# Performance work log

Measured on AMD Instinct MI355X. Metric: run time of the kernel, lower is better.

Reference implementation:

```python
import jax, jax.numpy as jnp
import numpy as np

B, CIN, COUT, H, W = 8, 128, 256, 256, 256


def setup_inputs() -> dict:
    key = jax.random.key(0)
    ks = jax.random.split(key, 6)
    x = jax.random.normal(ks[0], (B, CIN, H, W), dtype=jnp.float32)
    # conv weight [out, in, 3, 3]
    weight = jax.random.normal(ks[1], (COUT, CIN, 3, 3), dtype=jnp.float32) * 0.1
    move0_bias = jax.random.normal(ks[2], (1, CIN, 1, 1), dtype=jnp.float32) * 0.01
    pr_bias0 = jax.random.normal(ks[3], (1, COUT, 1, 1), dtype=jnp.float32) * 0.01
    prelu_alpha = jnp.full((COUT,), 0.25, dtype=jnp.float32)  # PyTorch PReLU default init
    pr_bias1 = jax.random.normal(ks[4], (1, COUT, 1, 1), dtype=jnp.float32) * 0.01
    return {"x": x, "weight": weight, "move0_bias": move0_bias,
            "pr_bias0": pr_bias0, "prelu_alpha": prelu_alpha, "pr_bias1": pr_bias1}


def _binary_activation(x):
    # STE: forward sign(x), backward grad of clip(x, -1, 1)
    clipped = jnp.clip(x, -1.0, 1.0)
    return jax.lax.stop_gradient(jnp.sign(x) - clipped) + clipped


def _binarize_weights(w):
    # per-output-filter scale: mean |w| over (in, kh, kw), detached
    scale = jax.lax.stop_gradient(jnp.mean(jnp.abs(w), axis=(1, 2, 3), keepdims=True))
    clipped = jnp.clip(w, -1.0, 1.0)
    return jax.lax.stop_gradient(scale * jnp.sign(w) - clipped) + clipped


def reference(x, weight, move0_bias, pr_bias0, prelu_alpha, pr_bias1):
    b, c, h, w = x.shape
    # AvgPool2d(kernel=2, stride=2)
    out = x.reshape(b, c, h // 2, 2, w // 2, 2).mean(axis=(3, 5))
    # LearnableBias
    out = out + move0_bias
    # BinaryActivation (sign with STE)
    out = _binary_activation(out)
    # HardBinaryConv 3x3, pad 1, stride 1, no bias
    bw = _binarize_weights(weight)
    y = jax.lax.conv_general_dilated(
        out, bw, window_strides=(1, 1), padding=((1, 1), (1, 1)),
        dimension_numbers=("NCHW", "OIHW", "NCHW"))
    # RPReLU: bias0 -> PReLU -> bias1
    y = y + pr_bias0
    y = jnp.where(y >= 0, y, prelu_alpha.reshape(1, -1, 1, 1) * y)
    y = y + pr_bias1
    return y
```

## Files before the change

### kernel.cpp

```cpp
#include <hip/hip_runtime.h>
#include <stdint.h>


__global__ __launch_bounds__(128) void wprep_kernel(const float* __restrict__ w,
                                                    uint32_t* __restrict__ packedW,
                                                    float* __restrict__ scaleW,
                                                    int* __restrict__ popcW) {
    int oc = blockIdx.x;
    int cin = threadIdx.x;
    const float* wp = w + ((long)oc * 128 + cin) * 9;
    float wk[9];
    float sabs = 0.f;
#pragma unroll
    for (int k = 0; k < 9; ++k) { wk[k] = wp[k]; sabs += fabsf(wk[k]); }
    int gi = cin >> 6;
    int lane = cin & 63;
    __shared__ float ssum[2];
    __shared__ int spc[2][9];
    for (int off = 32; off > 0; off >>= 1) sabs += __shfl_down(sabs, off, 64);
    if (lane == 0) ssum[gi] = sabs;
#pragma unroll
    for (int k = 0; k < 9; ++k) {
        unsigned long long m = __ballot(wk[k] > 0.f);
        if (lane == 0) {
            packedW[(oc * 9 + k) * 4 + 2 * gi]     = (uint32_t)m;
            packedW[(oc * 9 + k) * 4 + 2 * gi + 1] = (uint32_t)(m >> 32);
            spc[gi][k] = __popcll(m);
        }
    }
    __syncthreads();
    if (cin == 0) scaleW[oc] = (ssum[0] + ssum[1]) * (1.0f / 1152.0f);
    if (cin < 9) popcW[oc * 9 + cin] = spc[0][cin] + spc[1][cin];
}

__global__ __launch_bounds__(256) void pool_pack_kernel(const float* __restrict__ x,
                                                        const float* __restrict__ bias,
                                                        uint32_t* __restrict__ packedA) {
    int h = blockIdx.x;
    int b = blockIdx.y;
    int tid = threadIdx.x;
    __shared__ float sbias[128];
    __shared__ uint8_t sb[128 * 132];
    if (tid < 128) sbias[tid] = bias[tid];
    __syncthreads();
    const float4* x4 = reinterpret_cast<const float4*>(x);
#pragma unroll 4
    for (int it = 0; it < 32; ++it) {
        int j = it * 256 + tid;
        int c = j >> 6;
        int wq = j & 63;
        long base = ((long)(b * 128 + c) * 256 + 2 * h) * 64 + wq;
        float4 f0 = x4[base];
        float4 f1 = x4[base + 64];
        float p0 = (f0.x + f0.y + f1.x + f1.y) * 0.25f + sbias[c];
        float p1 = (f0.z + f0.w + f1.z + f1.w) * 0.25f + sbias[c];
        uint16_t v = (uint16_t)((p0 > 0.f ? 1u : 0u) | ((p1 > 0.f ? 1u : 0u) << 8));
        *reinterpret_cast<uint16_t*>(&sb[c * 132 + 2 * wq]) = v;
    }
    __syncthreads();
#pragma unroll
    for (int it = 0; it < 2; ++it) {
        int idx = it * 256 + tid;
        int q = idx & 3;
        int w = idx >> 2;
        uint32_t word = 0;
#pragma unroll
        for (int i = 0; i < 32; ++i)
            word |= ((uint32_t)sb[(32 * q + i) * 132 + w]) << i;
        packedA[(((long)b * 128 + h) * 128 + w) * 4 + q] = word;
    }
}

__global__ __launch_bounds__(256, 3) void conv_kernel(const uint32_t* __restrict__ packedA,
                                                      const uint32_t* __restrict__ packedW,
                                                      const float* __restrict__ scaleW,
                                                      const int* __restrict__ popcW,
                                                      const float* __restrict__ pb0,
                                                      const float* __restrict__ alpha,
                                                      const float* __restrict__ pb1,
                                                      float* __restrict__ out) {
    int h = blockIdx.x;
    int b = blockIdx.y;
    int tid = threadIdx.x;
    __shared__ uint32_t wlds[256 * 36];
    __shared__ uint4 alds[3][130];
    for (int i = tid; i < 256 * 36; i += 256) wlds[i] = packedW[i];
    for (int i = tid; i < 3 * 130; i += 256) {
        int r = i / 130, col = i % 130;
        int hh = h - 1 + r;
        uint4 v = make_uint4(0u, 0u, 0u, 0u);
        if (col >= 1 && col <= 128 && hh >= 0 && hh < 128) {
            const uint4* pa = reinterpret_cast<const uint4*>(packedA);
            v = pa[((long)b * 128 + hh) * 128 + (col - 1)];
        }
        alds[r][col] = v;
    }
    __syncthreads();

    int wv = tid >> 6;
    int lane = tid & 63;
    int px0 = lane;
    int px1 = lane + 64;

    uint4 a0[9], a1[9];
#pragma unroll
    for (int r = 0; r < 3; ++r)
#pragma unroll
        for (int dx = 0; dx < 3; ++dx) {
            a0[r * 3 + dx] = alds[r][px0 + dx];
            a1[r * 3 + dx] = alds[r][px1 + dx];
        }

    int inv0 = 0, inv1 = 0;
    if (h == 0)   { inv0 |= 0007; inv1 |= 0007; }
    if (h == 127) { inv0 |= 0700; inv1 |= 0700; }
    if (px0 == 0)   inv0 |= 0111;
    if (px1 == 127) inv1 |= 0444;

    long obase = (long)b * 256 * 128 * 128 + (long)h * 128;
    for (int oci = 0; oci < 64; ++oci) {
        int oc = wv * 64 + oci;
        const uint32_t* wp = &wlds[oc * 36];
        int p0a = 0, p0b = 0, p1a = 0, p1b = 0;
#pragma unroll
        for (int t = 0; t < 9; ++t) {
            uint4 wt = *reinterpret_cast<const uint4*>(&wp[t * 4]);
            p0a += __builtin_popcount(a0[t].x ^ wt.x) + __builtin_popcount(a0[t].y ^ wt.y);
            p0b += __builtin_popcount(a0[t].z ^ wt.z) + __builtin_popcount(a0[t].w ^ wt.w);
            p1a += __builtin_popcount(a1[t].x ^ wt.x) + __builtin_popcount(a1[t].y ^ wt.y);
            p1b += __builtin_popcount(a1[t].z ^ wt.z) + __builtin_popcount(a1[t].w ^ wt.w);
        }
        int t0 = 9 * 128 - 2 * (p0a + p0b);
        int t1 = 9 * 128 - 2 * (p1a + p1b);
        if (inv0) {
#pragma unroll
            for (int t = 0; t < 9; ++t)
                if ((inv0 >> t) & 1) t0 -= 128 - 2 * popcW[oc * 9 + t];
        }
        if (inv1) {
#pragma unroll
            for (int t = 0; t < 9; ++t)
                if ((inv1 >> t) & 1) t1 -= 128 - 2 * popcW[oc * 9 + t];
        }
        float s = scaleW[oc], b0v = pb0[oc], al = alpha[oc], b1v = pb1[oc];
        float y0 = s * (float)t0 + b0v;
        y0 = (y0 >= 0.f) ? y0 : al * y0;
        y0 += b1v;
        float y1 = s * (float)t1 + b0v;
        y1 = (y1 >= 0.f) ? y1 : al * y1;
        y1 += b1v;
        long o = obase + (long)oc * 128 * 128;
        out[o + px0] = y0;
        out[o + px1] = y1;
    }
}

extern "C" void kernel_launch(void* const* d_in, const int* in_sizes, int n_in,
                              void* d_out, int out_size, void* d_ws, size_t ws_size,
                              hipStream_t stream) {
    const float* x          = (const float*)d_in[0];
    const float* weight     = (const float*)d_in[1];
    const float* move0_bias = (const float*)d_in[2];
    const float* pb0        = (const float*)d_in[3];
    const float* alpha      = (const float*)d_in[4];
    const float* pb1        = (const float*)d_in[5];
    float* out = (float*)d_out;

    char* ws = (char*)d_ws;
    uint32_t* packedA = (uint32_t*)ws;
    uint32_t* packedW = (uint32_t*)(ws + 2097152);
    float*    scaleW  = (float*)  (ws + 2097152 + 36864);
    int*      popcW   = (int*)    (ws + 2097152 + 36864 + 1024);

    wprep_kernel<<<256, 128, 0, stream>>>(weight, packedW, scaleW, popcW);
    pool_pack_kernel<<<dim3(128, 8), 256, 0, stream>>>(x, move0_bias, packedA);
    conv_kernel<<<dim3(128, 8), 256, 0, stream>>>(packedA, packedW, scaleW, popcW,
                                                  pb0, alpha, pb1, out);
}
```

Measured before the change: 570.4 us.

## Tile conv as 2x2 output pixels per thread and split output channels across blocks

The conv kernel now computes a 2x2 output patch per thread from a 4x4 register window, so each weight uint4 read from shared memory is reused four times instead of twice. The grid is reshaped to (64 row-pairs, 2 channel halves, batch), which shrinks the per-block weight footprint and raises the occupancy hint to 4. Border corrections are precomputed per output channel as nine case sums in the weight prep kernel, and the epilogue constants are packed into a float4, removing branchy per-tap global loads. Output stores become float2 writes, which may be less coalesced than the earlier contiguous scalar stores across lanes.

```diff
diff --git a/kernel.cpp b/kernel.cpp
--- a/kernel.cpp
+++ b/kernel.cpp
@@ -3,9 +3,12 @@
 
 
 __global__ __launch_bounds__(128) void wprep_kernel(const float* __restrict__ w,
+                                                    const float* __restrict__ pb0,
+                                                    const float* __restrict__ alpha,
+                                                    const float* __restrict__ pb1,
                                                     uint32_t* __restrict__ packedW,
-                                                    float* __restrict__ scaleW,
-                                                    int* __restrict__ popcW) {
+                                                    int* __restrict__ corrCase,
+                                                    float4* __restrict__ epi) {
     int oc = blockIdx.x;
     int cin = threadIdx.x;
     const float* wp = w + ((long)oc * 128 + cin) * 9;
@@ -29,8 +32,29 @@
         }
     }
     __syncthreads();
-    if (cin == 0) scaleW[oc] = (ssum[0] + ssum[1]) * (1.0f / 1152.0f);
-    if (cin < 9) popcW[oc * 9 + cin] = spc[0][cin] + spc[1][cin];
+    if (cin == 0) {
+        float s = (ssum[0] + ssum[1]) * (1.0f / 1152.0f);
+        epi[oc] = make_float4(s, pb0[oc], alpha[oc], pb1[oc]);
+        int ct[9];
+#pragma unroll
+        for (int t = 0; t < 9; ++t) ct[t] = 128 - 2 * (spc[0][t] + spc[1][t]);
+        int cT = ct[0] + ct[1] + ct[2];
+        int cB = ct[6] + ct[7] + ct[8];
+        int cL = ct[0] + ct[3] + ct[6];
+        int cR = ct[2] + ct[5] + ct[8];
+        int cc[9];
+        cc[0] = 0;
+        cc[1] = cL;
+        cc[2] = cR;
+        cc[3] = cT;
+        cc[4] = cT + cL - ct[0];
+        cc[5] = cT + cR - ct[2];
+        cc[6] = cB;
+        cc[7] = cB + cL - ct[6];
+        cc[8] = cB + cR - ct[8];
+#pragma unroll
+        for (int k = 0; k < 9; ++k) corrCase[oc * 9 + k] = cc[k];
+    }
 }
 
 __global__ __launch_bounds__(256) void pool_pack_kernel(const float* __restrict__ x,
@@ -71,87 +95,88 @@
     }
 }
 
-__global__ __launch_bounds__(256, 3) void conv_kernel(const uint32_t* __restrict__ packedA,
+__device__ __forceinline__ int popc4(uint4 a, uint4 w) {
+    return __builtin_popcount(a.x ^ w.x) + __builtin_popcount(a.y ^ w.y) +
+           __builtin_popcount(a.z ^ w.z) + __builtin_popcount(a.w ^ w.w);
+}
+
+__global__ __launch_bounds__(256, 4) void conv_kernel(const uint32_t* __restrict__ packedA,
                                                       const uint32_t* __restrict__ packedW,
-                                                      const float* __restrict__ scaleW,
-                                                      const int* __restrict__ popcW,
-                                                      const float* __restrict__ pb0,
-                                                      const float* __restrict__ alpha,
-                                                      const float* __restrict__ pb1,
+                                                      const int* __restrict__ corrCase,
+                                                      const float4* __restrict__ epi,
                                                       float* __restrict__ out) {
-    int h = blockIdx.x;
-    int b = blockIdx.y;
+    int hp  = blockIdx.x;
+    int och = blockIdx.y;
+    int b   = blockIdx.z;
     int tid = threadIdx.x;
-    __shared__ uint32_t wlds[256 * 36];
-    __shared__ uint4 alds[3][130];
-    for (int i = tid; i < 256 * 36; i += 256) wlds[i] = packedW[i];
-    for (int i = tid; i < 3 * 130; i += 256) {
-        int r = i / 130, col = i % 130;
-        int hh = h - 1 + r;
+    int ocbase = och * 128;
+
+    __shared__ uint4 wlds[128 * 9];
+    __shared__ uint4 alds[4][132];
+    __shared__ int   clds[128 * 9];
+    __shared__ float4 elds[128];
+
+    const uint4* pw4 = reinterpret_cast<const uint4*>(packedW);
+    for (int i = tid; i < 128 * 9; i += 256) wlds[i] = pw4[ocbase * 9 + i];
+    const uint4* pa4 = reinterpret_cast<const uint4*>(packedA);
+    for (int i = tid; i < 4 * 132; i += 256) {
+        int r = i / 132, c = i % 132;
+        int hh = 2 * hp - 1 + r;
+        int col = c - 1;
         uint4 v = make_uint4(0u, 0u, 0u, 0u);
-        if (col >= 1 && col <= 128 && hh >= 0 && hh < 128) {
-            const uint4* pa = reinterpret_cast<const uint4*>(packedA);
-            v = pa[((long)b * 128 + hh) * 128 + (col - 1)];
-        }
-        alds[r][col] = v;
-    }
-    __syncthreads();
-
-    int wv = tid >> 6;
-    int lane = tid & 63;
-    int px0 = lane;
-    int px1 = lane + 64;
-
-    uint4 a0[9], a1[9];
-#pragma unroll
-    for (int r = 0; r < 3; ++r)
-#pragma unroll
-        for (int dx = 0; dx < 3; ++dx) {
-            a0[r * 3 + dx] = alds[r][px0 + dx];
-            a1[r * 3 + dx] = alds[r][px1 + dx];
-        }
-
-    int inv0 = 0, inv1 = 0;
-    if (h == 0)   { inv0 |= 0007; inv1 |= 0007; }
-    if (h == 127) { inv0 |= 0700; inv1 |= 0700; }
-    if (px0 == 0)   inv0 |= 0111;
-    if (px1 == 127) inv1 |= 0444;
-
-    long obase = (long)b * 256 * 128 * 128 + (long)h * 128;
-    for (int oci = 0; oci < 64; ++oci) {
-        int oc = wv * 64 + oci;
-        const uint32_t* wp = &wlds[oc * 36];
-        int p0a = 0, p0b = 0, p1a = 0, p1b = 0;
-#pragma unroll
-        for (int t = 0; t < 9; ++t) {
-            uint4 wt = *reinterpret_cast<const uint4*>(&wp[t * 4]);
-            p0a += __builtin_popcount(a0[t].x ^ wt.x) + __builtin_popcount(a0[t].y ^ wt.y);
-            p0b += __builtin_popcount(a0[t].z ^ wt.z) + __builtin_popcount(a0[t].w ^ wt.w);
-            p1a += __builtin_popcount(a1[t].x ^ wt.x) + __builtin_popcount(a1[t].y ^ wt.y);
-            p1b += __builtin_popcount(a1[t].z ^ wt.z) + __builtin_popcount(a1[t].w ^ wt.w);
-        }
-        int t0 = 9 * 128 - 2 * (p0a + p0b);
-        int t1 = 9 * 128 - 2 * (p1a + p1b);
-        if (inv0) {
-#pragma unroll
-            for (int t = 0; t < 9; ++t)
-                if ((inv0 >> t) & 1) t0 -= 128 - 2 * popcW[oc * 9 + t];
-        }
-        if (inv1) {
-#pragma unroll
-            for (int t = 0; t < 9; ++t)
-                if ((inv1 >> t) & 1) t1 -= 128 - 2 * popcW[oc * 9 + t];
-        }
-        float s = scaleW[oc], b0v = pb0[oc], al = alpha[oc], b1v = pb1[oc];
-        float y0 = s * (float)t0 + b0v;
-        y0 = (y0 >= 0.f) ? y0 : al * y0;
-        y0 += b1v;
-        float y1 = s * (float)t1 + b0v;
-        y1 = (y1 >= 0.f) ? y1 : al * y1;
-        y1 += b1v;
-        long o = obase + (long)oc * 128 * 128;
-        out[o + px0] = y0;
-        out[o + px1] = y1;
+        if (col >= 0 && col < 128 && hh >= 0 && hh < 128)
+            v = pa4[((b * 128 + hh) << 7) + col];
+        alds[r][c] = v;
+    }
+    for (int i = tid; i < 128 * 9; i += 256) clds[i] = corrCase[ocbase * 9 + i];
+    if (tid < 128) elds[tid] = epi[ocbase + tid];
+    __syncthreads();
+
+    int wv = tid >> 6, lane = tid & 63;
+    int w0 = 2 * lane;
+    uint4 A[4][4];
+#pragma unroll
+    for (int rr = 0; rr < 4; ++rr)
+#pragma unroll
+        for (int cc = 0; cc < 4; ++cc)
+            A[rr][cc] = alds[rr][w0 + cc];
+    __builtin_amdgcn_sched_barrier(0);
+
+    int r0 = 2 * hp, r1 = r0 + 1;
+    int hB0 = (r0 == 0)   ? 3 : 0;
+    int hB1 = (r1 == 127) ? 6 : 0;
+    int wBl = (lane == 0)  ? 1 : 0;
+    int wBr = (lane == 63) ? 2 : 0;
+    int c00 = hB0 + wBl, c01 = hB0 + wBr;
+    int c10 = hB1 + wBl, c11 = hB1 + wBr;
+
+    for (int i = 0; i < 32; ++i) {
+        int ocl = wv * 32 + i;
+        const uint4* wp = &wlds[ocl * 9];
+        int a00 = 0, a01 = 0, a10 = 0, a11 = 0;
+#pragma unroll
+        for (int r = 0; r < 3; ++r)
+#pragma unroll
+            for (int d = 0; d < 3; ++d) {
+                uint4 wt = wp[r * 3 + d];
+                a00 += popc4(A[r][d],         wt);
+                a01 += popc4(A[r][d + 1],     wt);
+                a10 += popc4(A[r + 1][d],     wt);
+                a11 += popc4(A[r + 1][d + 1], wt);
+            }
+        int cb = ocl * 9;
+        int t00 = 1152 - 2 * a00 - clds[cb + c00];
+        int t01 = 1152 - 2 * a01 - clds[cb + c01];
+        int t10 = 1152 - 2 * a10 - clds[cb + c10];
+        int t11 = 1152 - 2 * a11 - clds[cb + c11];
+        float4 e = elds[ocl];
+        float y00 = e.x * (float)t00 + e.y; y00 = (y00 >= 0.f) ? y00 : e.z * y00; y00 += e.w;
+        float y01 = e.x * (float)t01 + e.y; y01 = (y01 >= 0.f) ? y01 : e.z * y01; y01 += e.w;
+        float y10 = e.x * (float)t10 + e.y; y10 = (y10 >= 0.f) ? y10 : e.z * y10; y10 += e.w;
+        float y11 = e.x * (float)t11 + e.y; y11 = (y11 >= 0.f) ? y11 : e.z * y11; y11 += e.w;
+        long ob = (((long)(b * 256 + ocbase + ocl) * 128 + r0) << 7) + w0;
+        *reinterpret_cast<float2*>(out + ob)       = make_float2(y00, y01);
+        *reinterpret_cast<float2*>(out + ob + 128) = make_float2(y10, y11);
     }
 }
 
@@ -167,13 +192,13 @@
     float* out = (float*)d_out;
 
     char* ws = (char*)d_ws;
-    uint32_t* packedA = (uint32_t*)ws;
-    uint32_t* packedW = (uint32_t*)(ws + 2097152);
-    float*    scaleW  = (float*)  (ws + 2097152 + 36864);
-    int*      popcW   = (int*)    (ws + 2097152 + 36864 + 1024);
-
-    wprep_kernel<<<256, 128, 0, stream>>>(weight, packedW, scaleW, popcW);
+    uint32_t* packedA  = (uint32_t*)ws;
+    uint32_t* packedW  = (uint32_t*)(ws + 2097152);
+    int*      corrCase = (int*)     (ws + 2097152 + 36864);
+    float4*   epi      = (float4*)  (ws + 2097152 + 36864 + 9216);
+
+    wprep_kernel<<<256, 128, 0, stream>>>(weight, pb0, alpha, pb1,
+                                          packedW, corrCase, epi);
     pool_pack_kernel<<<dim3(128, 8), 256, 0, stream>>>(x, move0_bias, packedA);
-    conv_kernel<<<dim3(128, 8), 256, 0, stream>>>(packedA, packedW, scaleW, popcW,
-                                                  pb0, alpha, pb1, out);
-}
+    conv_kernel<<<dim3(64, 2, 8), 256, 0, stream>>>(packedA, packedW, corrCase, epi, out);
+}
```

After: 854.1 us. 1.5x slower.
